# Performance work log

Hardware: AMD Instinct MI355X
Metric: run time of the kernel (lower is better)

The kernel has to match this reference:

```python
import jax, jax.numpy as jnp
import numpy as np

B, N, F, H, L = 8, 512, 32, 64, 2

def setup_inputs() -> dict:
    key = jax.random.key(0)
    ks = jax.random.split(key, 16)
    s = lambda fan_in: 1.0 / np.sqrt(fan_in)
    return {
        "x": jax.random.normal(ks[0], (B, N, F), dtype=jnp.float32),
        # node encoder: Linear(F, H), stored as [in, out]
        "W_enc": jax.random.uniform(ks[1], (F, H), minval=-s(F), maxval=s(F)),
        "b_enc": jax.random.uniform(ks[2], (H,), minval=-s(F), maxval=s(F)),
        # edge MLP: Linear(2H, H) then Linear(H, 1)
        "W_e1": jax.random.uniform(ks[3], (2 * H, H), minval=-s(2 * H), maxval=s(2 * H)),
        "b_e1": jax.random.uniform(ks[4], (H,), minval=-s(2 * H), maxval=s(2 * H)),
        "W_e2": jax.random.uniform(ks[5], (H,), minval=-s(H), maxval=s(H)),
        "b_e2": jax.random.uniform(ks[6], (), minval=-s(H), maxval=s(H)),
        # per-layer message Linear(H, H)
        "W_msg": jax.random.uniform(ks[7], (L, H, H), minval=-s(H), maxval=s(H)),
        "b_msg": jax.random.uniform(ks[8], (L, H), minval=-s(H), maxval=s(H)),
        # per-layer GRUCell(H, H): gates ordered [r, z, n], stored as [in, 3H]
        "W_ih": jax.random.uniform(ks[9], (L, H, 3 * H), minval=-s(H), maxval=s(H)),
        "b_ih": jax.random.uniform(ks[10], (L, 3 * H), minval=-s(H), maxval=s(H)),
        "W_hh": jax.random.uniform(ks[11], (L, H, 3 * H), minval=-s(H), maxval=s(H)),
        "b_hh": jax.random.uniform(ks[12], (L, 3 * H), minval=-s(H), maxval=s(H)),
        # output Linear(H, 1)
        "W_out": jax.random.uniform(ks[13], (H, 1), minval=-s(H), maxval=s(H)),
        "b_out": jax.random.uniform(ks[14], (1,), minval=-s(H), maxval=s(H)),
    }

def reference(x, W_enc, b_enc, W_e1, b_e1, W_e2, b_e2, W_msg, b_msg,
              W_ih, b_ih, W_hh, b_hh, W_out, b_out):
    # Node encoding (dropout is eval-mode identity)
    h = jax.nn.relu(x @ W_enc + b_enc)  # [B, N, H]

    # Edge MLP on pairwise concat [h_i, h_j]: split W_e1 so we never build the 2H concat
    Wa, Wb = W_e1[:H], W_e1[H:]
    zi = h @ Wa                           # contribution of h_i, [B, N, H]
    zj = h @ Wb                           # contribution of h_j, [B, N, H]
    e = jax.nn.relu(zi[:, :, None, :] + zj[:, None, :, :] + b_e1)  # [B, N, N, H]
    logits = jnp.einsum('bijh,h->bij', e, W_e2) + b_e2             # [B, N, N]

    eye = jnp.eye(logits.shape[-1], dtype=bool)
    logits = jnp.where(eye[None], -jnp.inf, logits)
    adj = jax.nn.softmax(logits, axis=-1)
    adj = jnp.nan_to_num(adj, nan=0.0, posinf=0.0, neginf=0.0)

    for l in range(L):
        m = jnp.einsum('bij,bjh->bih', adj, h)             # message aggregation
        m = jax.nn.relu(m @ W_msg[l] + b_msg[l])
        # GRUCell update (gates [r, z, n])
        gi = m @ W_ih[l] + b_ih[l]
        gh = h @ W_hh[l] + b_hh[l]
        ir, iz, inn = jnp.split(gi, 3, axis=-1)
        hr, hz, hn = jnp.split(gh, 3, axis=-1)
        r = jax.nn.sigmoid(ir + hr)
        z = jax.nn.sigmoid(iz + hz)
        n = jnp.tanh(inn + r * hn)
        h = (1.0 - z) * n + z * h

    graph_emb = jnp.mean(h, axis=1)       # [B, H]
    return graph_emb @ W_out + b_out      # [B, 1]
```

## Files before the change

### kernel.cpp

```cpp
#include <hip/hip_runtime.h>
#include <math.h>

#define BB 8
#define NN 512
#define FF 32
#define HH 64
#define NEG_BIG (-1.0e30f)

__device__ __forceinline__ float lane_bcast(float v, int l) {
    return __int_as_float(__builtin_amdgcn_readlane(__float_as_int(v), l));
}

__global__ __launch_bounds__(256) void encode_kernel(
    const float* __restrict__ x, const float* __restrict__ W_enc,
    const float* __restrict__ b_enc, const float* __restrict__ W_e1,
    const float* __restrict__ b_e1,
    float* __restrict__ h, float* __restrict__ zi, float* __restrict__ zjT2)
{
    const int t = threadIdx.x;
    const int hh = t & 63;
    const int qu = __builtin_amdgcn_readfirstlane(t >> 6);
    const int gR = blockIdx.x * 4 + qu;

    const float xv = x[gR * FF + (hh & 31)];
    float acc = b_enc[hh];
#pragma unroll 8
    for (int k = 0; k < FF; ++k)
        acc = fmaf(lane_bcast(xv, k), W_enc[k * HH + hh], acc);
    const float hval = fmaxf(acc, 0.f);
    h[gR * HH + hh] = hval;

    float z1 = b_e1[hh], z2 = 0.f;
#pragma unroll 8
    for (int k = 0; k < HH; ++k) {
        const float hk = lane_bcast(hval, k);
        z1 = fmaf(hk, W_e1[k * HH + hh], z1);
        z2 = fmaf(hk, W_e1[(HH + k) * HH + hh], z2);
    }
    zi[gR * HH + hh] = z1;
    const int b = gR >> 9, n = gR & (NN - 1);
    zjT2[(((size_t)b * 32 + (hh >> 1)) * NN + n) * 2 + (hh & 1)] = z2;
}

template <int MODE>
__global__ __launch_bounds__(512, 8) void adjlayer_kernel(
    const float* __restrict__ zi, const float* __restrict__ zjT2,
    const float* __restrict__ We2, const float* __restrict__ be2,
    float* __restrict__ adjw, const float* __restrict__ adjr,
    const float* __restrict__ h_in,
    const float* __restrict__ Wmsg, const float* __restrict__ bmsg,
    const float* __restrict__ Wih, const float* __restrict__ bih,
    const float* __restrict__ Whh, const float* __restrict__ bhh,
    float* __restrict__ h_out, float* __restrict__ partial)
{
    const int b  = blockIdx.x >> 7;
    const int i0 = (blockIdx.x & 127) << 2;
    const int t  = threadIdx.x;
    const int tj = t & 63;
    const int w  = __builtin_amdgcn_readfirstlane(t >> 6);
    const int gR0 = b * NN + i0;
    const int j   = 64 * w + tj;

    __shared__ float smem[3168];
    __shared__ float mml[4][66];
    __shared__ float hol[4][66];
    __shared__ float redm[8][4], reds[8][4];
#define RED(p, r, c)        smem[(((p) * 4) + (r)) * 66 + (c)]
#define GP(h2, k2, r, g, c) smem[(((((h2) * 2 + (k2)) * 4 + (r)) * 3 + (g)) * 66) + (c)]

    if (w < 4) hol[w][tj] = h_in[(size_t)(gR0 + w) * HH + tj];

    float va[4];
    if (MODE == 0) {
        const float2* zi2 = (const float2*)(zi + (size_t)gR0 * HH);
        const float2* we2 = (const float2*)We2;
        const float2* zt2 = (const float2*)zjT2 + (size_t)b * 32 * NN + j;

        float2 a2[4];
#pragma unroll
        for (int r = 0; r < 4; ++r) a2[r] = make_float2(0.f, 0.f);
#pragma unroll 8
        for (int k2 = 0; k2 < 32; ++k2) {
            const float2 z = zt2[(size_t)k2 * NN];
            const float2 wk = we2[k2];
#pragma unroll
            for (int r = 0; r < 4; ++r) {
                const float2 zv = zi2[r * 32 + k2];
                a2[r].x = fmaf(fmaxf(zv.x + z.x, 0.f), wk.x, a2[r].x);
                a2[r].y = fmaf(fmaxf(zv.y + z.y, 0.f), wk.y, a2[r].y);
            }
        }
        const float bias2 = be2[0];
        float acc[4];
#pragma unroll
        for (int r = 0; r < 4; ++r) {
            acc[r] = a2[r].x + a2[r].y + bias2;
            if (j == i0 + r) acc[r] = NEG_BIG;
        }

#pragma unroll
        for (int r = 0; r < 4; ++r) {
            float m = acc[r];
#pragma unroll
            for (int off = 32; off >= 1; off >>= 1)
                m = fmaxf(m, __shfl_xor(m, off));
            if (tj == 0) redm[w][r] = m;
        }
        __syncthreads();
        float M[4];
#pragma unroll
        for (int r = 0; r < 4; ++r) {
            float m = redm[0][r];
#pragma unroll
            for (int p = 1; p < 8; ++p) m = fmaxf(m, redm[p][r]);
            M[r] = m;
        }
#pragma unroll
        for (int r = 0; r < 4; ++r) {
            va[r] = __expf(acc[r] - M[r]);
            float s = va[r];
#pragma unroll
            for (int off = 32; off >= 1; off >>= 1) s += __shfl_xor(s, off);
            if (tj == 0) reds[w][r] = s;
        }
        __syncthreads();
#pragma unroll
        for (int r = 0; r < 4; ++r) {
            float s = reds[0][r];
#pragma unroll
            for (int p = 1; p < 8; ++p) s += reds[p][r];
            va[r] *= 1.0f / s;
            adjw[(size_t)(gR0 + r) * NN + j] = va[r];
        }
    }

    {
        const float* hq = h_in + ((size_t)b * NN + 64 * w) * HH + tj;
        float mac[4] = {0.f, 0.f, 0.f, 0.f};
        if (MODE == 0) {
#pragma unroll 4
            for (int jj = 0; jj < 64; ++jj) {
                const float hv = hq[(size_t)jj * HH];
#pragma unroll
                for (int r = 0; r < 4; ++r)
                    mac[r] = fmaf(lane_bcast(va[r], jj), hv, mac[r]);
            }
        } else {
            const float* a0 = adjr + (size_t)(gR0 + 0) * NN + 64 * w;
            const float* a1 = adjr + (size_t)(gR0 + 1) * NN + 64 * w;
            const float* a2 = adjr + (size_t)(gR0 + 2) * NN + 64 * w;
            const float* a3 = adjr + (size_t)(gR0 + 3) * NN + 64 * w;
#pragma unroll 8
            for (int jj = 0; jj < 64; ++jj) {
                const float hv = hq[(size_t)jj * HH];
                mac[0] = fmaf(a0[jj], hv, mac[0]);
                mac[1] = fmaf(a1[jj], hv, mac[1]);
                mac[2] = fmaf(a2[jj], hv, mac[2]);
                mac[3] = fmaf(a3[jj], hv, mac[3]);
            }
        }
#pragma unroll
        for (int r = 0; r < 4; ++r) RED(w, r, tj) = mac[r];
    }
    __syncthreads();

    if (w < 4) {
        float m = RED(0, w, tj);
#pragma unroll
        for (int p = 1; p < 8; ++p) m += RED(p, w, tj);
        float mmv = bmsg[tj];
#pragma unroll 8
        for (int k = 0; k < HH; ++k)
            mmv = fmaf(lane_bcast(m, k), Wmsg[k * HH + tj], mmv);
        mml[w][tj] = fmaxf(mmv, 0.f);
    }
    __syncthreads();

    {
        const int half = w >> 2, kh = (w >> 1) & 1, rq = w & 1;
        const float* Wg = half ? Whh : Wih;
        const float* bg = half ? bhh : bih;
        float sreg[2];
#pragma unroll
        for (int r = 0; r < 2; ++r)
            sreg[r] = half ? hol[rq * 2 + r][tj] : mml[rq * 2 + r][tj];
        float g0[2], g1[2], g2[2];
#pragma unroll
        for (int r = 0; r < 2; ++r) {
            g0[r] = kh ? 0.f : bg[tj];
            g1[r] = kh ? 0.f : bg[64 + tj];
            g2[r] = kh ? 0.f : bg[128 + tj];
        }
        const int k0 = kh * 32;
#pragma unroll 4
        for (int kk = 0; kk < 32; ++kk) {
            const float* wk = Wg + (size_t)(k0 + kk) * 192;
            const float w0 = wk[tj], w1 = wk[64 + tj], w2 = wk[128 + tj];
#pragma unroll
            for (int r = 0; r < 2; ++r) {
                const float s = lane_bcast(sreg[r], k0 + kk);
                g0[r] = fmaf(s, w0, g0[r]);
                g1[r] = fmaf(s, w1, g1[r]);
                g2[r] = fmaf(s, w2, g2[r]);
            }
        }
#pragma unroll
        for (int r = 0; r < 2; ++r) {
            GP(half, kh, rq * 2 + r, 0, tj) = g0[r];
            GP(half, kh, rq * 2 + r, 1, tj) = g1[r];
            GP(half, kh, rq * 2 + r, 2, tj) = g2[r];
        }
    }
    __syncthreads();

    float hnew = 0.f;
    if (w < 4) {
        const float ir  = GP(0, 0, w, 0, tj) + GP(0, 1, w, 0, tj);
        const float iz  = GP(0, 0, w, 1, tj) + GP(0, 1, w, 1, tj);
        const float inn = GP(0, 0, w, 2, tj) + GP(0, 1, w, 2, tj);
        const float hr  = GP(1, 0, w, 0, tj) + GP(1, 1, w, 0, tj);
        const float hz  = GP(1, 0, w, 1, tj) + GP(1, 1, w, 1, tj);
        const float hn  = GP(1, 0, w, 2, tj) + GP(1, 1, w, 2, tj);
        const float rg = 1.f / (1.f + __expf(-(ir + hr)));
        const float zg = 1.f / (1.f + __expf(-(iz + hz)));
        const float ng = tanhf(inn + rg * hn);
        hnew = (1.f - zg) * ng + zg * hol[w][tj];
        h_out[(size_t)(gR0 + w) * HH + tj] = hnew;
    }

    if (MODE == 1) {
        __syncthreads();
        if (w < 4) mml[w][tj] = hnew;
        __syncthreads();
        if (w == 0) {
            partial[blockIdx.x * 64 + tj] =
                mml[0][tj] + mml[1][tj] + mml[2][tj] + mml[3][tj];
        }
    }
#undef RED
#undef GP
}

__global__ __launch_bounds__(64) void readout_kernel(
    const float* __restrict__ partial, const float* __restrict__ W_out,
    const float* __restrict__ b_out, float* __restrict__ out)
{
    const int b = blockIdx.x;
    const int hh = threadIdx.x;
    float s = 0.f;
#pragma unroll 8
    for (int c = 0; c < 128; ++c)
        s += partial[(b * 128 + c) * 64 + hh];
    float v = s * (1.0f / NN) * W_out[hh];
#pragma unroll
    for (int off = 32; off >= 1; off >>= 1) v += __shfl_xor(v, off);
    if (hh == 0) out[b] = v + b_out[0];
}

extern "C" void kernel_launch(void* const* d_in, const int* in_sizes, int n_in,
                              void* d_out, int out_size, void* d_ws, size_t ws_size,
                              hipStream_t stream)
{
    const float* x     = (const float*)d_in[0];
    const float* W_enc = (const float*)d_in[1];
    const float* b_enc = (const float*)d_in[2];
    const float* W_e1  = (const float*)d_in[3];
    const float* b_e1  = (const float*)d_in[4];
    const float* W_e2  = (const float*)d_in[5];
    const float* b_e2  = (const float*)d_in[6];
    const float* W_msg = (const float*)d_in[7];
    const float* b_msg = (const float*)d_in[8];
    const float* W_ih  = (const float*)d_in[9];
    const float* b_ih  = (const float*)d_in[10];
    const float* W_hh  = (const float*)d_in[11];
    const float* b_hh  = (const float*)d_in[12];
    const float* W_out = (const float*)d_in[13];
    const float* b_out = (const float*)d_in[14];
    float* out = (float*)d_out;

    float* ws   = (float*)d_ws;
    float* h0   = ws;
    float* h1   = h0 + BB * NN * HH;
    float* zi   = h1 + BB * NN * HH;
    float* zjT2 = zi + BB * NN * HH;
    float* prt  = zjT2 + BB * NN * HH;
    float* adjw = prt + 1024 * 64;

    encode_kernel<<<BB * NN / 4, 256, 0, stream>>>(
        x, W_enc, b_enc, W_e1, b_e1, h0, zi, zjT2);

    adjlayer_kernel<0><<<BB * (NN / 4), 512, 0, stream>>>(
        zi, zjT2, W_e2, b_e2, adjw, adjw, h0,
        W_msg, b_msg, W_ih, b_ih, W_hh, b_hh, h1, nullptr);
    adjlayer_kernel<1><<<BB * (NN / 4), 512, 0, stream>>>(
        zi, zjT2, W_e2, b_e2, adjw, adjw, h1,
        W_msg + HH * HH, b_msg + HH,
        W_ih + HH * 3 * HH, b_ih + 3 * HH, W_hh + HH * 3 * HH, b_hh + 3 * HH,
        h0, prt);

    readout_kernel<<<BB, 64, 0, stream>>>(prt, W_out, b_out, out);
}
```

Measured before the change: 72.78 us.

## Split adjacency softmax into own kernel and fuse readout via atomics

Moves the edge-MLP/softmax computation out of the first layer kernel into a dedicated adj_kernel, so both GRU layers use the same layer kernel reading adjacency from global memory. The separate readout kernel is removed: the last layer reduces its rows, scales by W_out and atomically adds into the output, which adj_kernel initialises with b_out. This may reduce register pressure in each kernel and drops the partial buffer. In exchange, layer 0 now re-reads adjacency from memory instead of using it from registers, and the kernel count stays the same.

```diff
diff --git a/kernel.cpp b/kernel.cpp
--- a/kernel.cpp
+++ b/kernel.cpp
@@ -42,16 +42,11 @@
     zjT2[(((size_t)b * 32 + (hh >> 1)) * NN + n) * 2 + (hh & 1)] = z2;
 }
 
-template <int MODE>
-__global__ __launch_bounds__(512, 8) void adjlayer_kernel(
+__global__ __launch_bounds__(512, 8) void adj_kernel(
     const float* __restrict__ zi, const float* __restrict__ zjT2,
     const float* __restrict__ We2, const float* __restrict__ be2,
-    float* __restrict__ adjw, const float* __restrict__ adjr,
-    const float* __restrict__ h_in,
-    const float* __restrict__ Wmsg, const float* __restrict__ bmsg,
-    const float* __restrict__ Wih, const float* __restrict__ bih,
-    const float* __restrict__ Whh, const float* __restrict__ bhh,
-    float* __restrict__ h_out, float* __restrict__ partial)
+    const float* __restrict__ b_out,
+    float* __restrict__ adjw, float* __restrict__ out)
 {
     const int b  = blockIdx.x >> 7;
     const int i0 = (blockIdx.x & 127) << 2;
@@ -61,103 +56,110 @@
     const int gR0 = b * NN + i0;
     const int j   = 64 * w + tj;
 
+    __shared__ float redm[8][4], reds[8][4];
+
+    if (blockIdx.x < BB && t == 0) out[blockIdx.x] = b_out[0];
+
+    const float2* zi2 = (const float2*)(zi + (size_t)gR0 * HH);
+    const float2* we2 = (const float2*)We2;
+    const float2* zt2 = (const float2*)zjT2 + (size_t)b * 32 * NN + j;
+
+    float2 a2[4];
+#pragma unroll
+    for (int r = 0; r < 4; ++r) a2[r] = make_float2(0.f, 0.f);
+#pragma unroll 8
+    for (int k2 = 0; k2 < 32; ++k2) {
+        const float2 z = zt2[(size_t)k2 * NN];
+        const float2 wk = we2[k2];
+#pragma unroll
+        for (int r = 0; r < 4; ++r) {
+            const float2 zv = zi2[r * 32 + k2];
+            a2[r].x = fmaf(fmaxf(zv.x + z.x, 0.f), wk.x, a2[r].x);
+            a2[r].y = fmaf(fmaxf(zv.y + z.y, 0.f), wk.y, a2[r].y);
+        }
+    }
+    const float bias2 = be2[0];
+    float acc[4];
+#pragma unroll
+    for (int r = 0; r < 4; ++r) {
+        acc[r] = a2[r].x + a2[r].y + bias2;
+        if (j == i0 + r) acc[r] = NEG_BIG;
+    }
+
+#pragma unroll
+    for (int r = 0; r < 4; ++r) {
+        float m = acc[r];
+#pragma unroll
+        for (int off = 32; off >= 1; off >>= 1)
+            m = fmaxf(m, __shfl_xor(m, off));
+        if (tj == 0) redm[w][r] = m;
+    }
+    __syncthreads();
+    float M[4];
+#pragma unroll
+    for (int r = 0; r < 4; ++r) {
+        float m = redm[0][r];
+#pragma unroll
+        for (int p = 1; p < 8; ++p) m = fmaxf(m, redm[p][r]);
+        M[r] = m;
+    }
+    float e[4];
+#pragma unroll
+    for (int r = 0; r < 4; ++r) {
+        e[r] = __expf(acc[r] - M[r]);
+        float s = e[r];
+#pragma unroll
+        for (int off = 32; off >= 1; off >>= 1) s += __shfl_xor(s, off);
+        if (tj == 0) reds[w][r] = s;
+    }
+    __syncthreads();
+#pragma unroll
+    for (int r = 0; r < 4; ++r) {
+        float s = reds[0][r];
+#pragma unroll
+        for (int p = 1; p < 8; ++p) s += reds[p][r];
+        adjw[(size_t)(gR0 + r) * NN + j] = e[r] * (1.0f / s);
+    }
+}
+
+template <int LAST>
+__global__ __launch_bounds__(512, 8) void layer_kernel(
+    const float* __restrict__ adjr, const float* __restrict__ h_in,
+    const float* __restrict__ Wmsg, const float* __restrict__ bmsg,
+    const float* __restrict__ Wih, const float* __restrict__ bih,
+    const float* __restrict__ Whh, const float* __restrict__ bhh,
+    const float* __restrict__ Wout,
+    float* __restrict__ h_out, float* __restrict__ out)
+{
+    const int b  = blockIdx.x >> 7;
+    const int i0 = (blockIdx.x & 127) << 2;
+    const int t  = threadIdx.x;
+    const int tj = t & 63;
+    const int w  = __builtin_amdgcn_readfirstlane(t >> 6);
+    const int gR0 = b * NN + i0;
+
     __shared__ float smem[3168];
     __shared__ float mml[4][66];
     __shared__ float hol[4][66];
-    __shared__ float redm[8][4], reds[8][4];
 #define RED(p, r, c)        smem[(((p) * 4) + (r)) * 66 + (c)]
 #define GP(h2, k2, r, g, c) smem[(((((h2) * 2 + (k2)) * 4 + (r)) * 3 + (g)) * 66) + (c)]
 
     if (w < 4) hol[w][tj] = h_in[(size_t)(gR0 + w) * HH + tj];
 
-    float va[4];
-    if (MODE == 0) {
-        const float2* zi2 = (const float2*)(zi + (size_t)gR0 * HH);
-        const float2* we2 = (const float2*)We2;
-        const float2* zt2 = (const float2*)zjT2 + (size_t)b * 32 * NN + j;
-
-        float2 a2[4];
-#pragma unroll
-        for (int r = 0; r < 4; ++r) a2[r] = make_float2(0.f, 0.f);
-#pragma unroll 8
-        for (int k2 = 0; k2 < 32; ++k2) {
-            const float2 z = zt2[(size_t)k2 * NN];
-            const float2 wk = we2[k2];
-#pragma unroll
-            for (int r = 0; r < 4; ++r) {
-                const float2 zv = zi2[r * 32 + k2];
-                a2[r].x = fmaf(fmaxf(zv.x + z.x, 0.f), wk.x, a2[r].x);
-                a2[r].y = fmaf(fmaxf(zv.y + z.y, 0.f), wk.y, a2[r].y);
-            }
-        }
-        const float bias2 = be2[0];
-        float acc[4];
-#pragma unroll
-        for (int r = 0; r < 4; ++r) {
-            acc[r] = a2[r].x + a2[r].y + bias2;
-            if (j == i0 + r) acc[r] = NEG_BIG;
-        }
-
-#pragma unroll
-        for (int r = 0; r < 4; ++r) {
-            float m = acc[r];
-#pragma unroll
-            for (int off = 32; off >= 1; off >>= 1)
-                m = fmaxf(m, __shfl_xor(m, off));
-            if (tj == 0) redm[w][r] = m;
-        }
-        __syncthreads();
-        float M[4];
-#pragma unroll
-        for (int r = 0; r < 4; ++r) {
-            float m = redm[0][r];
-#pragma unroll
-            for (int p = 1; p < 8; ++p) m = fmaxf(m, redm[p][r]);
-            M[r] = m;
-        }
-#pragma unroll
-        for (int r = 0; r < 4; ++r) {
-            va[r] = __expf(acc[r] - M[r]);
-            float s = va[r];
-#pragma unroll
-            for (int off = 32; off >= 1; off >>= 1) s += __shfl_xor(s, off);
-            if (tj == 0) reds[w][r] = s;
-        }
-        __syncthreads();
-#pragma unroll
-        for (int r = 0; r < 4; ++r) {
-            float s = reds[0][r];
-#pragma unroll
-            for (int p = 1; p < 8; ++p) s += reds[p][r];
-            va[r] *= 1.0f / s;
-            adjw[(size_t)(gR0 + r) * NN + j] = va[r];
-        }
-    }
-
     {
         const float* hq = h_in + ((size_t)b * NN + 64 * w) * HH + tj;
+        const float* a0 = adjr + (size_t)(gR0 + 0) * NN + 64 * w;
+        const float* a1 = adjr + (size_t)(gR0 + 1) * NN + 64 * w;
+        const float* a2 = adjr + (size_t)(gR0 + 2) * NN + 64 * w;
+        const float* a3 = adjr + (size_t)(gR0 + 3) * NN + 64 * w;
         float mac[4] = {0.f, 0.f, 0.f, 0.f};
-        if (MODE == 0) {
-#pragma unroll 4
-            for (int jj = 0; jj < 64; ++jj) {
-                const float hv = hq[(size_t)jj * HH];
-#pragma unroll
-                for (int r = 0; r < 4; ++r)
-                    mac[r] = fmaf(lane_bcast(va[r], jj), hv, mac[r]);
-            }
-        } else {
-            const float* a0 = adjr + (size_t)(gR0 + 0) * NN + 64 * w;
-            const float* a1 = adjr + (size_t)(gR0 + 1) * NN + 64 * w;
-            const float* a2 = adjr + (size_t)(gR0 + 2) * NN + 64 * w;
-            const float* a3 = adjr + (size_t)(gR0 + 3) * NN + 64 * w;
-#pragma unroll 8
-            for (int jj = 0; jj < 64; ++jj) {
-                const float hv = hq[(size_t)jj * HH];
-                mac[0] = fmaf(a0[jj], hv, mac[0]);
-                mac[1] = fmaf(a1[jj], hv, mac[1]);
-                mac[2] = fmaf(a2[jj], hv, mac[2]);
-                mac[3] = fmaf(a3[jj], hv, mac[3]);
-            }
+#pragma unroll 8
+        for (int jj = 0; jj < 64; ++jj) {
+            const float hv = hq[(size_t)jj * HH];
+            mac[0] = fmaf(a0[jj], hv, mac[0]);
+            mac[1] = fmaf(a1[jj], hv, mac[1]);
+            mac[2] = fmaf(a2[jj], hv, mac[2]);
+            mac[3] = fmaf(a3[jj], hv, mac[3]);
         }
 #pragma unroll
         for (int r = 0; r < 4; ++r) RED(w, r, tj) = mac[r];
@@ -228,33 +230,20 @@
         h_out[(size_t)(gR0 + w) * HH + tj] = hnew;
     }
 
-    if (MODE == 1) {
+    if (LAST) {
         __syncthreads();
         if (w < 4) mml[w][tj] = hnew;
         __syncthreads();
         if (w == 0) {
-            partial[blockIdx.x * 64 + tj] =
-                mml[0][tj] + mml[1][tj] + mml[2][tj] + mml[3][tj];
+            float v = (mml[0][tj] + mml[1][tj] + mml[2][tj] + mml[3][tj])
+                      * (1.0f / NN) * Wout[tj];
+#pragma unroll
+            for (int off = 32; off >= 1; off >>= 1) v += __shfl_xor(v, off);
+            if (tj == 0) atomicAdd(out + b, v);
         }
     }
 #undef RED
 #undef GP
-}
-
-__global__ __launch_bounds__(64) void readout_kernel(
-    const float* __restrict__ partial, const float* __restrict__ W_out,
-    const float* __restrict__ b_out, float* __restrict__ out)
-{
-    const int b = blockIdx.x;
-    const int hh = threadIdx.x;
-    float s = 0.f;
-#pragma unroll 8
-    for (int c = 0; c < 128; ++c)
-        s += partial[(b * 128 + c) * 64 + hh];
-    float v = s * (1.0f / NN) * W_out[hh];
-#pragma unroll
-    for (int off = 32; off >= 1; off >>= 1) v += __shfl_xor(v, off);
-    if (hh == 0) out[b] = v + b_out[0];
 }
 
 extern "C" void kernel_launch(void* const* d_in, const int* in_sizes, int n_in,
@@ -283,20 +272,18 @@
     float* h1   = h0 + BB * NN * HH;
     float* zi   = h1 + BB * NN * HH;
     float* zjT2 = zi + BB * NN * HH;
-    float* prt  = zjT2 + BB * NN * HH;
-    float* adjw = prt + 1024 * 64;
+    float* adjw = zjT2 + BB * NN * HH;
 
     encode_kernel<<<BB * NN / 4, 256, 0, stream>>>(
         x, W_enc, b_enc, W_e1, b_e1, h0, zi, zjT2);
 
-    adjlayer_kernel<0><<<BB * (NN / 4), 512, 0, stream>>>(
-        zi, zjT2, W_e2, b_e2, adjw, adjw, h0,
-        W_msg, b_msg, W_ih, b_ih, W_hh, b_hh, h1, nullptr);
-    adjlayer_kernel<1><<<BB * (NN / 4), 512, 0, stream>>>(
-        zi, zjT2, W_e2, b_e2, adjw, adjw, h1,
-        W_msg + HH * HH, b_msg + HH,
+    adj_kernel<<<BB * (NN / 4), 512, 0, stream>>>(
+        zi, zjT2, W_e2, b_e2, b_out, adjw, out);
+
+    layer_kernel<0><<<BB * (NN / 4), 512, 0, stream>>>(
+        adjw, h0, W_msg, b_msg, W_ih, b_ih, W_hh, b_hh, W_out, h1, out);
+    layer_kernel<1><<<BB * (NN / 4), 512, 0, stream>>>(
+        adjw, h1, W_msg + HH * HH, b_msg + HH,
         W_ih + HH * 3 * HH, b_ih + 3 * HH, W_hh + HH * 3 * HH, b_hh + 3 * HH,
-        h0, prt);
-
-    readout_kernel<<<BB, 64, 0, stream>>>(prt, W_out, b_out, out);
-}
+        W_out, h0, out);
+}
```

Result: no change. 72.19 us (-0.8%).
